# Optimization experiments

Hardware: AMD Instinct MI355X
Metric: run time of the kernel (lower is better)

The kernel has to match this reference:

```python
import math
import jax, jax.numpy as jnp
import numpy as np

N_HEADS = 16
TOPK_FACTOR = 0.5

def setup_inputs() -> dict:
    key = jax.random.key(0)
    ks = jax.random.split(key, 11)
    B, L, D = 2, 2048, 1024
    s = 0.02
    return {
        "q": jax.random.normal(ks[0], (B, L, D), jnp.float32),
        "k": jax.random.normal(ks[1], (B, L, D), jnp.float32),
        "v": jax.random.normal(ks[2], (B, L, D), jnp.float32),
        "Wq": jax.random.normal(ks[3], (D, D), jnp.float32) * s,
        "bq": jnp.zeros((D,), jnp.float32),
        "Wk": jax.random.normal(ks[4], (D, D), jnp.float32) * s,
        "bk": jnp.zeros((D,), jnp.float32),
        "Wv": jax.random.normal(ks[5], (D, D), jnp.float32) * s,
        "bv": jnp.zeros((D,), jnp.float32),
        "Wo": jax.random.normal(ks[6], (D, D), jnp.float32) * s,
        "bo": jnp.zeros((D,), jnp.float32),
    }

def reference(q, k, v, Wq, bq, Wk, bk, Wv, bv, Wo, bo):
    B, Lq, D = q.shape
    Lk = k.shape[1]
    H = N_HEADS
    d_k = D // H
    # projections -> [B, H, L, d_k]
    Q = (q @ Wq.T + bq).reshape(B, Lq, H, d_k).transpose(0, 2, 1, 3)
    K = (k @ Wk.T + bk).reshape(B, Lk, H, d_k).transpose(0, 2, 1, 3)
    V = (v @ Wv.T + bv).reshape(B, Lk, H, d_k).transpose(0, 2, 1, 3)
    # dense scores [B, H, Lq, Lk]
    scores = jnp.einsum("bhqd,bhkd->bhqk", Q, K) / math.sqrt(d_k)
    topk = max(1, int(TOPK_FACTOR * Lk))
    topk_scores, topk_idx = jax.lax.top_k(scores, topk)  # [B,H,Lq,topk]
    sm = jax.nn.softmax(topk_scores, axis=-1)
    # scatter softmax probs back into a zero [B,H,Lq,Lk] tensor (dropout in eval = identity)
    b_idx = jnp.arange(B)[:, None, None, None]
    h_idx = jnp.arange(H)[None, :, None, None]
    q_idx = jnp.arange(Lq)[None, None, :, None]
    attn = jnp.zeros_like(scores).at[b_idx, h_idx, q_idx, topk_idx].set(sm)
    ctx = jnp.einsum("bhqk,bhkd->bhqd", attn, V)
    ctx = ctx.transpose(0, 2, 1, 3).reshape(B, Lq, H * d_k)
    return ctx @ Wo.T + bo
```

## Files before the change

### kernel.cpp

```cpp
#include <hip/hip_runtime.h>
#include <math.h>

#define BATCH 2
#define SEQ 2048
#define DM 1024
#define NH 16
#define DH 64
#define TOPKN 1024
#define MROWS (BATCH * SEQ)

typedef float f32x4 __attribute__((ext_vector_type(4)));
typedef short s16x8 __attribute__((ext_vector_type(8)));
typedef short s16x4 __attribute__((ext_vector_type(4)));

#if __has_builtin(__builtin_amdgcn_mfma_f32_16x16x16_bf16)
#define MFMA1616(acc, a, b) acc = __builtin_amdgcn_mfma_f32_16x16x16_bf16(a, b, acc, 0, 0, 0)
#define MFMA1616_FENCE()
#elif __has_builtin(__builtin_amdgcn_mfma_f32_16x16x16bf16_1k)
#define MFMA1616(acc, a, b) acc = __builtin_amdgcn_mfma_f32_16x16x16bf16_1k(a, b, acc, 0, 0, 0)
#define MFMA1616_FENCE()
#else
#define MFMA1616(acc, a, b) \
  asm volatile("v_mfma_f32_16x16x16_bf16 %0, %1, %2, %0" : "+v"(acc) : "v"(a), "v"(b))
#define MFMA1616_FENCE() asm volatile("s_nop 7\ns_nop 7")
#endif

__device__ __forceinline__ unsigned short f2bf(float x) {
  unsigned u = __float_as_uint(x);
  return (unsigned short)((u + 0x7FFFu + ((u >> 16) & 1u)) >> 16);
}
__device__ __forceinline__ unsigned packHL(float x) {
  unsigned h = f2bf(x);
  float r = x - __uint_as_float(h << 16);
  unsigned l = f2bf(r);
  return h | (l << 16);
}
__device__ __forceinline__ unsigned hipair(float a, float b) {
  return __builtin_amdgcn_perm(__float_as_uint(b), __float_as_uint(a), 0x07060302u);
}
__device__ __forceinline__ unsigned lopair(float a, float b) {
  float ra = a - __uint_as_float(__float_as_uint(a) & 0xFFFF0000u);
  float rb = b - __uint_as_float(__float_as_uint(b) & 0xFFFF0000u);
  unsigned out;
  asm("v_cvt_pk_bf16_f32 %0, %1, %2" : "=v"(out) : "v"(ra), "v"(rb));
  return out;
}

__global__ __launch_bounds__(256) void convW(const float* __restrict__ W,
                                             unsigned short* __restrict__ Whi,
                                             unsigned short* __restrict__ Wlo) {
  int i = (blockIdx.x * 256 + threadIdx.x) * 4;
  float4 x = *(const float4*)&W[i];
  float xs[4] = {x.x, x.y, x.z, x.w};
  union { s16x4 v; unsigned short s[4]; } hu, lu;
#pragma unroll
  for (int e = 0; e < 4; ++e) {
    unsigned short hb = f2bf(xs[e]);
    hu.s[e] = hb;
    lu.s[e] = f2bf(xs[e] - __uint_as_float((unsigned)hb << 16));
  }
  *(s16x4*)&Whi[i] = hu.v;
  *(s16x4*)&Wlo[i] = lu.v;
}

template <int ASRC, int MODE>
__global__ __launch_bounds__(512) void gemm_mfma(
    const void* __restrict__ Asrc, const unsigned short* __restrict__ Whi,
    const unsigned short* __restrict__ Wlo, const float* __restrict__ bias,
    void* __restrict__ out0, void* __restrict__ out1) {
  __shared__ unsigned short Ah[128][64], Al[128][64];
  __shared__ unsigned short Bh[128][64], Bl[128][64];

  const int f = blockIdx.x;
  const int xcd = f & 7, r_ = f >> 3;
  const int bm = xcd * 4 + (r_ >> 3);
  const int bn = r_ & 7;
  const int m0g = bm * 128, n0g = bn * 128;
  const int t = threadIdx.x, w = t >> 6, lane = t & 63;
  const int g = lane >> 4, c = lane & 15;
  const int wm = w >> 2, wn = w & 3;

  f32x4 acc[4][2];
#pragma unroll
  for (int i = 0; i < 4; ++i)
#pragma unroll
    for (int j = 0; j < 2; ++j) acc[i][j] = (f32x4){0.f, 0.f, 0.f, 0.f};

#pragma unroll 1
  for (int k0 = 0; k0 < 1024; k0 += 64) {
#pragma unroll
    for (int i = 0; i < 2; ++i) {
      int oid = t * 2 + i;
      int rr = oid >> 3, j = oid & 7;
      unsigned hw[4], lw[4];
      if (ASRC == 0) {
        const float* src = (const float*)Asrc + (size_t)(m0g + rr) * 1024 + k0 + j * 8;
        float4 x0 = *(const float4*)src, x1 = *(const float4*)(src + 4);
        float xs[8] = {x0.x, x0.y, x0.z, x0.w, x1.x, x1.y, x1.z, x1.w};
#pragma unroll
        for (int p = 0; p < 4; ++p) {
          hw[p] = hipair(xs[2 * p], xs[2 * p + 1]);
          lw[p] = lopair(xs[2 * p], xs[2 * p + 1]);
        }
      } else {
        const unsigned* src = (const unsigned*)Asrc + (size_t)(m0g + rr) * 1024 + k0 + j * 8;
        uint4 u0 = *(const uint4*)src, u1 = *(const uint4*)(src + 4);
        unsigned us[8] = {u0.x, u0.y, u0.z, u0.w, u1.x, u1.y, u1.z, u1.w};
#pragma unroll
        for (int p = 0; p < 4; ++p) {
          hw[p] = __builtin_amdgcn_perm(us[2 * p + 1], us[2 * p], 0x05040100u);
          lw[p] = __builtin_amdgcn_perm(us[2 * p + 1], us[2 * p], 0x07060302u);
        }
      }
      int od = (j ^ (rr & 7)) * 8;
      *(uint4*)&Ah[rr][od] = make_uint4(hw[0], hw[1], hw[2], hw[3]);
      *(uint4*)&Al[rr][od] = make_uint4(lw[0], lw[1], lw[2], lw[3]);
    }
#pragma unroll
    for (int i = 0; i < 4; ++i) {
      int oid = t * 4 + i;
      int pl = oid >> 10, idx = oid & 1023, rr = idx >> 3, j = idx & 7;
      const unsigned short* src = (pl ? Wlo : Whi) + (size_t)(n0g + rr) * 1024 + k0 + j * 8;
      uint4 d = *(const uint4*)src;
      int od = (j ^ (rr & 7)) * 8;
      if (pl) *(uint4*)&Bl[rr][od] = d; else *(uint4*)&Bh[rr][od] = d;
    }
    __syncthreads();
#pragma unroll
    for (int k2 = 0; k2 < 2; ++k2) {
      s16x8 ah[4], al4[4], bh[2], bl[2];
      int ob = ((k2 * 4 + g) ^ (c & 7)) * 8;
#pragma unroll
      for (int i = 0; i < 4; ++i) {
        int rr = wm * 64 + i * 16 + c;
        ah[i] = *(const s16x8*)&Ah[rr][ob];
        al4[i] = *(const s16x8*)&Al[rr][ob];
      }
#pragma unroll
      for (int j = 0; j < 2; ++j) {
        int rr = wn * 32 + j * 16 + c;
        bh[j] = *(const s16x8*)&Bh[rr][ob];
        bl[j] = *(const s16x8*)&Bl[rr][ob];
      }
#pragma unroll
      for (int i = 0; i < 4; ++i)
#pragma unroll
        for (int j = 0; j < 2; ++j) {
          acc[i][j] = __builtin_amdgcn_mfma_f32_16x16x32_bf16(ah[i], bh[j], acc[i][j], 0, 0, 0);
          acc[i][j] = __builtin_amdgcn_mfma_f32_16x16x32_bf16(ah[i], bl[j], acc[i][j], 0, 0, 0);
          acc[i][j] = __builtin_amdgcn_mfma_f32_16x16x32_bf16(al4[i], bh[j], acc[i][j], 0, 0, 0);
        }
    }
    __syncthreads();
  }

#pragma unroll
  for (int j = 0; j < 2; ++j) {
    const int col = n0g + wn * 32 + j * 16 + c;
    const float bj = bias[col];
#pragma unroll
    for (int i = 0; i < 4; ++i) {
      const int row0 = m0g + wm * 64 + i * 16 + g * 4;
      if (MODE == 0) {
        float* O = (float*)out0;
#pragma unroll
        for (int rr = 0; rr < 4; ++rr)
          O[(size_t)(row0 + rr) * 1024 + col] = acc[i][j][rr] + bj;
      } else if (MODE == 1) {
        unsigned* Q = (unsigned*)out0;
#pragma unroll
        for (int rr = 0; rr < 4; ++rr)
          Q[(size_t)(row0 + rr) * 1024 + col] = packHL((acc[i][j][rr] + bj) * 1024.0f);
      } else if (MODE == 2) {
        unsigned short* Khi = (unsigned short*)out0;
        unsigned short* Klo = (unsigned short*)out1;
#pragma unroll
        for (int rr = 0; rr < 4; ++rr) {
          float x = acc[i][j][rr] + bj;
          unsigned short hb = f2bf(x);
          Khi[(size_t)(row0 + rr) * 1024 + col] = hb;
          Klo[(size_t)(row0 + rr) * 1024 + col] = f2bf(x - __uint_as_float((unsigned)hb << 16));
        }
      } else {
        unsigned short* Vt = (unsigned short*)out0;
        int b = row0 >> 11, l0 = row0 & (SEQ - 1);
        int h = col >> 6, dh = col & 63;
        union { s16x4 v; unsigned short sh[4]; } vv;
#pragma unroll
        for (int rr = 0; rr < 4; ++rr) vv.sh[rr] = f2bf(acc[i][j][rr] + bj);
        *(s16x4*)&Vt[(((size_t)b * NH + h) * DH + dh) * SEQ + l0] = vv.v;
      }
    }
  }
}

__global__ __launch_bounds__(1024, 4) void attn_mfma(
    const unsigned* __restrict__ QHL, const unsigned short* __restrict__ Khi,
    const unsigned short* __restrict__ Klo, const unsigned short* __restrict__ Vt,
    unsigned* __restrict__ CtxP) {
  __shared__ __align__(16) char smem[16 * 32 * 66 * 4];
  __shared__ __align__(16) float szum[32][16];
  __shared__ unsigned Tlds[32];
  unsigned (*sc)[1028] = (unsigned(*)[1028])smem;
  float (*ctxp)[32][66] = (float(*)[32][66])smem;

  int wg = blockIdx.x;
  wg = (wg & 7) * 256 + (wg >> 3);
  const int bh = wg >> 6, qt = wg & 63;
  const int b = bh >> 4, h = bh & 15;
  const int q0 = qt * 32;
  const int t = threadIdx.x, wid = t >> 6, lane = t & 63;
  const int g = lane >> 4, c = lane & 15;
  const size_t rowb = (size_t)b * SEQ;

  s16x8 qhiA[2], qloA[2], qhiB[2], qloB[2];
#pragma unroll
  for (int qh = 0; qh < 2; ++qh) {
    const unsigned* qp = QHL + (rowb + q0 + qh * 16 + c) * DM + h * DH + g * 8;
#pragma unroll
    for (int ds = 0; ds < 2; ++ds) {
      unsigned uw[8];
      *(uint4*)&uw[0] = *(const uint4*)(qp + ds * 32);
      *(uint4*)&uw[4] = *(const uint4*)(qp + ds * 32 + 4);
      union { s16x8 v; unsigned u[4]; } hi_, lo_;
#pragma unroll
      for (int p = 0; p < 4; ++p) {
        hi_.u[p] = (uw[2 * p] & 0xFFFFu) | (uw[2 * p + 1] << 16);
        lo_.u[p] = (uw[2 * p] >> 16) | (uw[2 * p + 1] & 0xFFFF0000u);
      }
      if (qh == 0) { qhiA[ds] = hi_.v; qloA[ds] = lo_.v; }
      else         { qhiB[ds] = hi_.v; qloB[ds] = lo_.v; }
    }
  }

  unsigned pkA[8][2], pkB[8][2];
  {
    const f32x4 INIT = (f32x4){32768.5f, 32768.5f, 32768.5f, 32768.5f};
    const size_t kcol = (size_t)h * DH + g * 8;
#pragma unroll
    for (int tt = 0; tt < 8; ++tt) {
      const size_t krow = (rowb + wid * 128 + tt * 16 + c) * DM + kcol;
      s16x8 kh0 = *(const s16x8*)(Khi + krow);
      s16x8 kh1 = *(const s16x8*)(Khi + krow + 32);
      s16x8 kl0 = *(const s16x8*)(Klo + krow);
      s16x8 kl1 = *(const s16x8*)(Klo + krow + 32);
      f32x4 aA = __builtin_amdgcn_mfma_f32_16x16x32_bf16(kh0, qhiA[0], INIT, 0, 0, 0);
      f32x4 aB = __builtin_amdgcn_mfma_f32_16x16x32_bf16(kh0, qhiB[0], INIT, 0, 0, 0);
      aA = __builtin_amdgcn_mfma_f32_16x16x32_bf16(kh1, qhiA[1], aA, 0, 0, 0);
      aB = __builtin_amdgcn_mfma_f32_16x16x32_bf16(kh1, qhiB[1], aB, 0, 0, 0);
      aA = __builtin_amdgcn_mfma_f32_16x16x32_bf16(kl0, qhiA[0], aA, 0, 0, 0);
      aB = __builtin_amdgcn_mfma_f32_16x16x32_bf16(kl0, qhiB[0], aB, 0, 0, 0);
      aA = __builtin_amdgcn_mfma_f32_16x16x32_bf16(kl1, qhiA[1], aA, 0, 0, 0);
      aB = __builtin_amdgcn_mfma_f32_16x16x32_bf16(kl1, qhiB[1], aB, 0, 0, 0);
      aA = __builtin_amdgcn_mfma_f32_16x16x32_bf16(kh0, qloA[0], aA, 0, 0, 0);
      aB = __builtin_amdgcn_mfma_f32_16x16x32_bf16(kh0, qloB[0], aB, 0, 0, 0);
      aA = __builtin_amdgcn_mfma_f32_16x16x32_bf16(kh1, qloA[1], aA, 0, 0, 0);
      aB = __builtin_amdgcn_mfma_f32_16x16x32_bf16(kh1, qloB[1], aB, 0, 0, 0);
      unsigned a0 = (unsigned)fminf(aA[0], 65535.f);
      unsigned a1 = (unsigned)fminf(aA[1], 65535.f);
      unsigned a2 = (unsigned)fminf(aA[2], 65535.f);
      unsigned a3 = (unsigned)fminf(aA[3], 65535.f);
      pkA[tt][0] = a0 | (a1 << 16);
      pkA[tt][1] = a2 | (a3 << 16);
      unsigned b0 = (unsigned)fminf(aB[0], 65535.f);
      unsigned b1 = (unsigned)fminf(aB[1], 65535.f);
      unsigned b2 = (unsigned)fminf(aB[2], 65535.f);
      unsigned b3 = (unsigned)fminf(aB[3], 65535.f);
      pkB[tt][0] = b0 | (b1 << 16);
      pkB[tt][1] = b2 | (b3 << 16);
    }
  }

#pragma unroll
  for (int tt = 0; tt < 8; ++tt) {
    int col = wid * 64 + tt * 8 + g * 2;
    *(uint2*)&sc[c][col] = make_uint2(pkA[tt][0], pkA[tt][1]);
    *(uint2*)&sc[c + 16][col] = make_uint2(pkB[tt][0], pkB[tt][1]);
  }
  __syncthreads();

  {
    const int r = 2 * wid + (lane >> 5);
    const int hl = lane & 31;
    uint4 ts[8];
#pragma unroll
    for (int i = 0; i < 8; ++i)
      ts[i] = *(const uint4*)&sc[r][hl * 4 + i * 128];

    unsigned lo = 30720u, hi = 34816u;
#pragma unroll 1
    for (int it = 0; it < 12; ++it) {
      const unsigned mid = (lo + hi) >> 1;
      int cnt = 0;
#pragma unroll
      for (int i = 0; i < 8; ++i) {
        unsigned a0 = ts[i].x, a1 = ts[i].y, a2 = ts[i].z, a3 = ts[i].w;
        cnt += ((a0 & 0xFFFFu) >= mid) ? 1 : 0;
        cnt += ((a0 >> 16) >= mid) ? 1 : 0;
        cnt += ((a1 & 0xFFFFu) >= mid) ? 1 : 0;
        cnt += ((a1 >> 16) >= mid) ? 1 : 0;
        cnt += ((a2 & 0xFFFFu) >= mid) ? 1 : 0;
        cnt += ((a2 >> 16) >= mid) ? 1 : 0;
        cnt += ((a3 & 0xFFFFu) >= mid) ? 1 : 0;
        cnt += ((a3 >> 16) >= mid) ? 1 : 0;
      }
      cnt += __shfl_xor(cnt, 1);
      cnt += __shfl_xor(cnt, 2);
      cnt += __shfl_xor(cnt, 4);
      cnt += __shfl_xor(cnt, 8);
      cnt += __shfl_xor(cnt, 16);
      bool ge = cnt >= TOPKN;
      lo = ge ? mid : lo;
      hi = ge ? hi : mid;
    }
    if ((lane & 31) == 0) Tlds[r] = lo;
  }
  __syncthreads();
  const unsigned TA = Tlds[c];
  const unsigned TB = Tlds[c + 16];

  const float C1 = 1.44269504f / 8192.0f;
  const float C2 = -49152.0f * (1.44269504f / 8192.0f);
  f32x4 opvA[4], opvB[4];
#pragma unroll
  for (int j = 0; j < 4; ++j) {
    opvA[j] = (f32x4){0.f, 0.f, 0.f, 0.f};
    opvB[j] = (f32x4){0.f, 0.f, 0.f, 0.f};
  }
  float zA = 0.f, zB = 0.f;
  {
    const unsigned short* vb0 = Vt + ((size_t)bh * DH + c) * SEQ + wid * 128 + g * 4;
#pragma unroll
    for (int kt = 0; kt < 8; ++kt) {
      unsigned pa0 = pkA[kt][0], pa1 = pkA[kt][1];
      unsigned ua0 = pa0 & 0xFFFFu, ua1 = pa0 >> 16;
      unsigned ua2 = pa1 & 0xFFFFu, ua3 = pa1 >> 16;
      float ea0 = (ua0 >= TA) ? exp2f(fmaf((float)ua0, C1, C2)) : 0.f;
      float ea1 = (ua1 >= TA) ? exp2f(fmaf((float)ua1, C1, C2)) : 0.f;
      float ea2 = (ua2 >= TA) ? exp2f(fmaf((float)ua2, C1, C2)) : 0.f;
      float ea3 = (ua3 >= TA) ? exp2f(fmaf((float)ua3, C1, C2)) : 0.f;
      zA += (ea0 + ea1) + (ea2 + ea3);
      union { s16x4 v; unsigned u[2]; } pbA;
      pbA.u[0] = ((__float_as_uint(ea0) + 0x8000u) >> 16) |
                 ((__float_as_uint(ea1) + 0x8000u) & 0xFFFF0000u);
      pbA.u[1] = ((__float_as_uint(ea2) + 0x8000u) >> 16) |
                 ((__float_as_uint(ea3) + 0x8000u) & 0xFFFF0000u);
      unsigned pb0 = pkB[kt][0], pb1 = pkB[kt][1];
      unsigned ub0 = pb0 & 0xFFFFu, ub1 = pb0 >> 16;
      unsigned ub2 = pb1 & 0xFFFFu, ub3 = pb1 >> 16;
      float eb0 = (ub0 >= TB) ? exp2f(fmaf((float)ub0, C1, C2)) : 0.f;
      float eb1 = (ub1 >= TB) ? exp2f(fmaf((float)ub1, C1, C2)) : 0.f;
      float eb2 = (ub2 >= TB) ? exp2f(fmaf((float)ub2, C1, C2)) : 0.f;
      float eb3 = (ub3 >= TB) ? exp2f(fmaf((float)ub3, C1, C2)) : 0.f;
      zB += (eb0 + eb1) + (eb2 + eb3);
      union { s16x4 v; unsigned u[2]; } pbB;
      pbB.u[0] = ((__float_as_uint(eb0) + 0x8000u) >> 16) |
                 ((__float_as_uint(eb1) + 0x8000u) & 0xFFFF0000u);
      pbB.u[1] = ((__float_as_uint(eb2) + 0x8000u) >> 16) |
                 ((__float_as_uint(eb3) + 0x8000u) & 0xFFFF0000u);
#pragma unroll
      for (int j = 0; j < 4; ++j) {
        s16x4 va = *(const s16x4*)(vb0 + (size_t)j * 16 * SEQ + kt * 16);
        MFMA1616(opvA[j], va, pbA.v);
        MFMA1616(opvB[j], va, pbB.v);
      }
    }
    MFMA1616_FENCE();
  }

  zA += __shfl_xor(zA, 16);
  zA += __shfl_xor(zA, 32);
  zB += __shfl_xor(zB, 16);
  zB += __shfl_xor(zB, 32);
  if (lane < 16) {
    szum[c][wid] = zA;
    szum[c + 16][wid] = zB;
  }
  __syncthreads();
#pragma unroll
  for (int j = 0; j < 4; ++j) {
    *(f32x4*)&ctxp[wid][c][j * 16 + g * 4] = opvA[j];
    *(f32x4*)&ctxp[wid][c + 16][j * 16 + g * 4] = opvB[j];
  }
  __syncthreads();

  if (t < 512) {
    const int q = t >> 4, d4 = t & 15;
    float4 z0 = *(float4*)&szum[q][0];
    float4 z1 = *(float4*)&szum[q][4];
    float4 z2 = *(float4*)&szum[q][8];
    float4 z3 = *(float4*)&szum[q][12];
    float rinv = 1.f / ((z0.x + z0.y + z0.z + z0.w) + (z1.x + z1.y + z1.z + z1.w) +
                        (z2.x + z2.y + z2.z + z2.w) + (z3.x + z3.y + z3.z + z3.w));
    f32x4 ssum = (f32x4){0.f, 0.f, 0.f, 0.f};
#pragma unroll
    for (int w2 = 0; w2 < 16; ++w2)
      ssum += *(const f32x4*)&ctxp[w2][q][d4 * 4];
    unsigned ov[4];
    ov[0] = packHL(ssum[0] * rinv);
    ov[1] = packHL(ssum[1] * rinv);
    ov[2] = packHL(ssum[2] * rinv);
    ov[3] = packHL(ssum[3] * rinv);
    *(uint4*)&CtxP[(rowb + q0 + q) * DM + h * DH + d4 * 4] = *(uint4*)&ov[0];
  }
}

extern "C" void kernel_launch(void* const* d_in, const int* in_sizes, int n_in,
                              void* d_out, int out_size, void* d_ws, size_t ws_size,
                              hipStream_t stream) {
  const float* q  = (const float*)d_in[0];
  const float* k  = (const float*)d_in[1];
  const float* v  = (const float*)d_in[2];
  const float* Wq = (const float*)d_in[3];
  const float* bq = (const float*)d_in[4];
  const float* Wk = (const float*)d_in[5];
  const float* bk = (const float*)d_in[6];
  const float* Wv = (const float*)d_in[7];
  const float* bv = (const float*)d_in[8];
  const float* Wo = (const float*)d_in[9];
  const float* bo = (const float*)d_in[10];
  float* out = (float*)d_out;

  char* ws = (char*)d_ws;
  unsigned* QHL       = (unsigned*)ws;
  unsigned short* Khi = (unsigned short*)(ws + (16u << 20));
  unsigned short* Klo = (unsigned short*)(ws + (24u << 20));
  unsigned short* Vt  = (unsigned short*)(ws + (32u << 20));
  unsigned short* Whi = (unsigned short*)(ws + (40u << 20));
  unsigned short* Wlo = (unsigned short*)(ws + (42u << 20));

  convW<<<1024, 256, 0, stream>>>(Wq, Whi, Wlo);
  gemm_mfma<0, 1><<<256, 512, 0, stream>>>(q, Whi, Wlo, bq, QHL, nullptr);
  convW<<<1024, 256, 0, stream>>>(Wk, Whi, Wlo);
  gemm_mfma<0, 2><<<256, 512, 0, stream>>>(k, Whi, Wlo, bk, Khi, Klo);
  convW<<<1024, 256, 0, stream>>>(Wv, Whi, Wlo);
  gemm_mfma<0, 3><<<256, 512, 0, stream>>>(v, Whi, Wlo, bv, Vt, nullptr);
  attn_mfma<<<BATCH * NH * (SEQ / 32), 1024, 0, stream>>>(QHL, Khi, Klo, Vt, QHL);
  convW<<<1024, 256, 0, stream>>>(Wo, Whi, Wlo);
  gemm_mfma<1, 0><<<256, 512, 0, stream>>>(QHL, Whi, Wlo, bo, out, nullptr);
}
```

Before: 602.6 us.

## Double-buffer K tiles into LDS via async global_load_lds and raise MFMA priority

The score loop no longer loads K hi/lo fragments straight from global memory into registers. Each wave now stages two 16-row K tiles ahead into a per-wave LDS double buffer with global_load_lds, uses vmcnt waits, and reads the fragments back from LDS, so global latency overlaps the MFMA work. It also wraps the QK and PV MFMA blocks in s_setprio(1) to favour matrix issue across waves. The risks are a hand-counted vmcnt that must stay exact, a new barrier before the score tile reuses the same shared memory, and a possible mismatch between the global_load_lds lane layout and the per-lane LDS read layout.

```diff
diff --git a/kernel.cpp b/kernel.cpp
--- a/kernel.cpp
+++ b/kernel.cpp
@@ -194,6 +194,24 @@
   }
 }
 
+#define STAGE_K(TT, BUF)                                                          \
+  do {                                                                            \
+    char* lb_ = (char*)smem + (size_t)wid * 8192 + (size_t)(BUF) * 4096;          \
+    const size_t o_ = (size_t)(TT) * 16 * DM;                                     \
+    __builtin_amdgcn_global_load_lds(                                             \
+        (const __attribute__((address_space(1))) void*)(kh0s + o_),               \
+        (__attribute__((address_space(3))) void*)(lb_), 16, 0, 0);                \
+    __builtin_amdgcn_global_load_lds(                                             \
+        (const __attribute__((address_space(1))) void*)(kh1s + o_),               \
+        (__attribute__((address_space(3))) void*)(lb_ + 1024), 16, 0, 0);         \
+    __builtin_amdgcn_global_load_lds(                                             \
+        (const __attribute__((address_space(1))) void*)(kl0s + o_),               \
+        (__attribute__((address_space(3))) void*)(lb_ + 2048), 16, 0, 0);         \
+    __builtin_amdgcn_global_load_lds(                                             \
+        (const __attribute__((address_space(1))) void*)(kl1s + o_),               \
+        (__attribute__((address_space(3))) void*)(lb_ + 3072), 16, 0, 0);         \
+  } while (0)
+
 __global__ __launch_bounds__(1024, 4) void attn_mfma(
     const unsigned* __restrict__ QHL, const unsigned short* __restrict__ Khi,
     const unsigned short* __restrict__ Klo, const unsigned short* __restrict__ Vt,
@@ -233,17 +251,29 @@
     }
   }
 
+  const int lrow = lane & 15, lchunk = lane >> 4;
+  const size_t ksrow = (rowb + (size_t)wid * 128 + lrow) * DM + (size_t)h * DH + lchunk * 8;
+  const unsigned short* kh0s = Khi + ksrow;
+  const unsigned short* kh1s = Khi + ksrow + 32;
+  const unsigned short* kl0s = Klo + ksrow;
+  const unsigned short* kl1s = Klo + ksrow + 32;
+
   unsigned pkA[8][2], pkB[8][2];
   {
     const f32x4 INIT = (f32x4){32768.5f, 32768.5f, 32768.5f, 32768.5f};
-    const size_t kcol = (size_t)h * DH + g * 8;
+    const unsigned short* lwave = (const unsigned short*)(smem + (size_t)wid * 8192) + lane * 8;
+    STAGE_K(0, 0);
+    STAGE_K(1, 1);
 #pragma unroll
     for (int tt = 0; tt < 8; ++tt) {
-      const size_t krow = (rowb + wid * 128 + tt * 16 + c) * DM + kcol;
-      s16x8 kh0 = *(const s16x8*)(Khi + krow);
-      s16x8 kh1 = *(const s16x8*)(Khi + krow + 32);
-      s16x8 kl0 = *(const s16x8*)(Klo + krow);
-      s16x8 kl1 = *(const s16x8*)(Klo + krow + 32);
+      if (tt < 7) asm volatile("s_waitcnt vmcnt(4)" ::: "memory");
+      else        asm volatile("s_waitcnt vmcnt(0)" ::: "memory");
+      const unsigned short* lb = lwave + (tt & 1) * 2048;
+      s16x8 kh0 = *(const s16x8*)(lb);
+      s16x8 kh1 = *(const s16x8*)(lb + 512);
+      s16x8 kl0 = *(const s16x8*)(lb + 1024);
+      s16x8 kl1 = *(const s16x8*)(lb + 1536);
+      __builtin_amdgcn_s_setprio(1);
       f32x4 aA = __builtin_amdgcn_mfma_f32_16x16x32_bf16(kh0, qhiA[0], INIT, 0, 0, 0);
       f32x4 aB = __builtin_amdgcn_mfma_f32_16x16x32_bf16(kh0, qhiB[0], INIT, 0, 0, 0);
       aA = __builtin_amdgcn_mfma_f32_16x16x32_bf16(kh1, qhiA[1], aA, 0, 0, 0);
@@ -256,6 +286,7 @@
       aB = __builtin_amdgcn_mfma_f32_16x16x32_bf16(kh0, qloB[0], aB, 0, 0, 0);
       aA = __builtin_amdgcn_mfma_f32_16x16x32_bf16(kh1, qloA[1], aA, 0, 0, 0);
       aB = __builtin_amdgcn_mfma_f32_16x16x32_bf16(kh1, qloB[1], aB, 0, 0, 0);
+      __builtin_amdgcn_s_setprio(0);
       unsigned a0 = (unsigned)fminf(aA[0], 65535.f);
       unsigned a1 = (unsigned)fminf(aA[1], 65535.f);
       unsigned a2 = (unsigned)fminf(aA[2], 65535.f);
@@ -268,8 +299,11 @@
       unsigned b3 = (unsigned)fminf(aB[3], 65535.f);
       pkB[tt][0] = b0 | (b1 << 16);
       pkB[tt][1] = b2 | (b3 << 16);
-    }
-  }
+      asm volatile("" ::: "memory");
+      if (tt < 6) STAGE_K(tt + 2, tt & 1);
+    }
+  }
+  __syncthreads();
 
 #pragma unroll
   for (int tt = 0; tt < 8; ++tt) {
@@ -358,12 +392,14 @@
                  ((__float_as_uint(eb1) + 0x8000u) & 0xFFFF0000u);
       pbB.u[1] = ((__float_as_uint(eb2) + 0x8000u) >> 16) |
                  ((__float_as_uint(eb3) + 0x8000u) & 0xFFFF0000u);
+      __builtin_amdgcn_s_setprio(1);
 #pragma unroll
       for (int j = 0; j < 4; ++j) {
         s16x4 va = *(const s16x4*)(vb0 + (size_t)j * 16 * SEQ + kt * 16);
         MFMA1616(opvA[j], va, pbA.v);
         MFMA1616(opvB[j], va, pbB.v);
       }
+      __builtin_amdgcn_s_setprio(0);
     }
     MFMA1616_FENCE();
   }
```

Result: no change. 612.1 us (+1.6%).
